# Performance work log

Hardware: AMD Instinct MI355X
Metric: run time of the kernel (lower is better)

The kernel has to match this reference:

```python
import jax, jax.numpy as jnp
import numpy as np

EMB_D, N_SLOTS, KEY_D, N_ITER = 768, 8, 128, 5
ATTN_EPS = 1e-8
LN_EPS = 1e-5


def layer_norm(x, g, b):
    mu = jnp.mean(x, axis=-1, keepdims=True)
    var = jnp.mean(jnp.square(x - mu), axis=-1, keepdims=True)
    return (x - mu) * jax.lax.rsqrt(var + LN_EPS) * g + b


def xavier(key, shape):
    fan_in, fan_out = shape[-1], shape[-2] if len(shape) > 1 else shape[-1]
    a = float(np.sqrt(6.0 / (fan_in + fan_out)))
    return jax.random.uniform(key, shape, jnp.float32, -a, a)


def setup_inputs() -> dict:
    key = jax.random.key(0)
    ks = jax.random.split(key, 24)
    B, N = 128, 196
    k = KEY_D
    inp = {
        "features": jax.random.normal(ks[0], (B, N, EMB_D), jnp.float32),
        "slot_noise": jax.random.normal(ks[1], (B, N_SLOTS, k), jnp.float32),
        # LayerNorms
        "ln_in_g": jnp.ones((EMB_D,), jnp.float32), "ln_in_b": jnp.zeros((EMB_D,), jnp.float32),
        "ln_slot_g": jnp.ones((k,), jnp.float32), "ln_slot_b": jnp.zeros((k,), jnp.float32),
        "ln_out_g": jnp.ones((k,), jnp.float32), "ln_out_b": jnp.zeros((k,), jnp.float32),
        "ln_dec_g": jnp.ones((k,), jnp.float32), "ln_dec_b": jnp.zeros((k,), jnp.float32),
        # slot prior
        "mu": xavier(ks[2], (1, 1, k)),
        "log_sigma": xavier(ks[3], (1, 1, k)),
        # projections (torch Linear weight layout: [out, in])
        "Wk": xavier(ks[4], (k, EMB_D)),
        "Wq": xavier(ks[5], (k, k)),
        "Wv": xavier(ks[6], (k, EMB_D)),
        # GRUCell
        "W_ih": jax.random.uniform(ks[7], (3 * k, k), jnp.float32, -1.0/np.sqrt(k), 1.0/np.sqrt(k)),
        "W_hh": jax.random.uniform(ks[8], (3 * k, k), jnp.float32, -1.0/np.sqrt(k), 1.0/np.sqrt(k)),
        "b_ih": jnp.zeros((3 * k,), jnp.float32),
        "b_hh": jnp.zeros((3 * k,), jnp.float32),
        # slot MLP
        "mlp_W1": xavier(ks[9], (k, k)), "mlp_b1": jnp.zeros((k,), jnp.float32),
        "mlp_W2": xavier(ks[10], (k, k)), "mlp_b2": jnp.zeros((k,), jnp.float32),
        # decoder
        "dec_W1": xavier(ks[11], (2 * k, k)), "dec_b1": jnp.zeros((2 * k,), jnp.float32),
        "dec_W2": xavier(ks[12], (EMB_D, 2 * k)), "dec_b2": jnp.zeros((EMB_D,), jnp.float32),
        "dec_W3": xavier(ks[13], (EMB_D, EMB_D)), "dec_b3": jnp.zeros((EMB_D,), jnp.float32),
    }
    return inp


def gru_cell(x, h, W_ih, W_hh, b_ih, b_hh):
    gi = x @ W_ih.T + b_ih  # [*, 3k]
    gh = h @ W_hh.T + b_hh
    ir, iz, inn = jnp.split(gi, 3, axis=-1)
    hr, hz, hn = jnp.split(gh, 3, axis=-1)
    r = jax.nn.sigmoid(ir + hr)
    z = jax.nn.sigmoid(iz + hz)
    n = jnp.tanh(inn + r * hn)
    return (1.0 - z) * n + z * h


def reference(features, slot_noise, ln_in_g, ln_in_b, ln_slot_g, ln_slot_b,
              ln_out_g, ln_out_b, ln_dec_g, ln_dec_b, mu, log_sigma,
              Wk, Wq, Wv, W_ih, W_hh, b_ih, b_hh,
              mlp_W1, mlp_b1, mlp_W2, mlp_b2,
              dec_W1, dec_b1, dec_W2, dec_b2, dec_W3, dec_b3):
    feats_ln = layer_norm(features, ln_in_g, ln_in_b)  # [B,N,E]
    slots = slot_noise * jnp.exp(log_sigma) + mu       # [B,K,D]
    k_proj = (feats_ln @ Wk.T) * (KEY_D ** -0.5)       # [B,N,D]
    v_proj = feats_ln @ Wv.T                           # [B,N,D]

    attn_vis = None
    for _ in range(N_ITER):
        slots_prev = slots
        s_ln = layer_norm(slots, ln_slot_g, ln_slot_b)
        q = s_ln @ Wq.T                                # [B,K,D]
        logits = jnp.einsum('bnd,bkd->bnk', k_proj, q)
        attn_vis = jax.nn.softmax(logits, axis=-1)     # softmax over slots
        attn = attn_vis + ATTN_EPS
        attn = attn / jnp.sum(attn, axis=-2, keepdims=True)  # normalize over tokens
        updates = jnp.einsum('bnk,bnd->bkd', attn, v_proj)
        slots = gru_cell(updates, slots_prev, W_ih, W_hh, b_ih, b_hh)
        h = jax.nn.relu(layer_norm(slots, ln_out_g, ln_out_b) @ mlp_W1.T + mlp_b1)
        slots = slots + (h @ mlp_W2.T + mlp_b2)

    sf = layer_norm(slots, ln_dec_g, ln_dec_b)
    sf = jax.nn.relu(sf @ dec_W1.T + dec_b1)
    sf = jax.nn.relu(sf @ dec_W2.T + dec_b2)
    sf = sf @ dec_W3.T + dec_b3                        # [B,K,E]
    recon = jnp.einsum('bkd,bnk->bnd', sf, attn_vis)   # [B,N,E]
    recon_loss = jnp.mean(jnp.square(recon - features))
    return slots, attn_vis, recon_loss
```

## Files before the change

kernel.cpp:

```cpp
#include <hip/hip_runtime.h>
#include <hip/hip_bf16.h>
#include <math.h>

#define B_    128
#define N_    196
#define E_    768
#define K_    8
#define D_    128
#define BNR   (B_*N_)
#define ITERS 5

#define OFF_PART   0
#define OFF_SDEC   512
#define OFF_WBF    66048
#define OFF_KPBF   647680
#define OFF_VPTBF  2351616
#define OFF_ABF    4186624

typedef __attribute__((ext_vector_type(8))) short bf16x8;
typedef __attribute__((ext_vector_type(4))) float f32x4;

#define MFMA16(a, b, c) __builtin_amdgcn_mfma_f32_16x16x32_bf16(a, b, c, 0, 0, 0)

__device__ __forceinline__ float wave_red_sum64(float v) {
    #pragma unroll
    for (int o = 32; o > 0; o >>= 1) v += __shfl_xor(v, o);
    return v;
}

__device__ __forceinline__ unsigned short f2bf(float v) {
    union { float f; unsigned int u; } c; c.f = v;
    unsigned int u = c.u + 0x7fffu + ((c.u >> 16) & 1u);
    return (unsigned short)(u >> 16);
}

__device__ __forceinline__ void gl_lds16(const void* g, void* l) {
    __builtin_amdgcn_global_load_lds(
        (const __attribute__((address_space(1))) unsigned int*)g,
        (__attribute__((address_space(3))) unsigned int*)l, 16, 0, 0);
}

__device__ __forceinline__ int swz128(int row, int j) {
    return row * 128 + ((((j >> 3) ^ (row & 7))) << 3) + (j & 7);
}
__device__ __forceinline__ int swz256(int row, int j) {
    return row * 256 + ((((j >> 3) ^ (row & 7))) << 3) + (j & 7);
}
__device__ __forceinline__ bf16x8 ldA128(const unsigned short* base, int fr, int kq, int ks) {
    int ch = (ks * 4 + kq) ^ (fr & 7);
    return *(const bf16x8*)(base + fr * 128 + ch * 8);
}
__device__ __forceinline__ bf16x8 ldA256(const unsigned short* base, int fr, int kq, int ks) {
    int ch = (ks * 4 + kq) ^ (fr & 7);
    return *(const bf16x8*)(base + fr * 256 + ch * 8);
}
__device__ __forceinline__ bf16x8 ldW128(const unsigned short* W, int row, int ks, int kq) {
    return *(const bf16x8*)(W + (size_t)row * 128 + ks * 32 + kq * 8);
}

struct WCEnt { const float* s; unsigned short* d; float scale; int t0; };
struct WCArgs { WCEnt m[10]; };

__global__ __launch_bounds__(256) void wconv_all(WCArgs a) {
    int bid = blockIdx.x, i = 0;
    #pragma unroll
    for (int j = 1; j < 10; ++j) if (bid >= a.m[j].t0) i = j;
    int off = (bid - a.m[i].t0) * 2048 + threadIdx.x * 8;
    const float* s = a.m[i].s + off;
    unsigned short* d = a.m[i].d + off;
    float sc = a.m[i].scale;
    float4 v0 = *(const float4*)s, v1 = *(const float4*)(s + 4);
    ushort4 o0, o1;
    o0.x = f2bf(v0.x * sc); o0.y = f2bf(v0.y * sc);
    o0.z = f2bf(v0.z * sc); o0.w = f2bf(v0.w * sc);
    o1.x = f2bf(v1.x * sc); o1.y = f2bf(v1.y * sc);
    o1.z = f2bf(v1.z * sc); o1.w = f2bf(v1.w * sc);
    *(ushort4*)d = o0; *(ushort4*)(d + 4) = o1;
}

__global__ __launch_bounds__(256) void padzero_k(unsigned short* kpb, unsigned short* vpt) {
    int i = blockIdx.x * 256 + threadIdx.x;
    ushort4 z = {0, 0, 0, 0};
    if (i < 49152) {
        int q = i * 4;
        int b = q / 1536, off = q - b * 1536;
        *(ushort4*)(kpb + ((size_t)b * 208 + 196) * 128 + off) = z;
    } else {
        int c = i - 49152;
        int bd = c / 7, cc = c - bd * 7;
        *(ushort4*)(vpt + (size_t)bd * 224 + 196 + cc * 4) = z;
    }
}

__global__ __launch_bounds__(256) void ln_bf16_k(const float* __restrict__ f,
                                                 const float* __restrict__ g,
                                                 const float* __restrict__ bv,
                                                 unsigned short* __restrict__ out) {
    int wid = blockIdx.x * 4 + (threadIdx.x >> 6);
    int lane = threadIdx.x & 63;
    const float* row = f + (size_t)wid * E_;
    float4 x[3];
    float s = 0.f, s2 = 0.f;
    #pragma unroll
    for (int c = 0; c < 3; ++c) {
        x[c] = *(const float4*)(row + c * 256 + lane * 4);
        s  += x[c].x + x[c].y + x[c].z + x[c].w;
        s2 += x[c].x * x[c].x + x[c].y * x[c].y + x[c].z * x[c].z + x[c].w * x[c].w;
    }
    s  = wave_red_sum64(s);
    s2 = wave_red_sum64(s2);
    float m = s * (1.f / E_);
    float rs = rsqrtf(s2 * (1.f / E_) - m * m + 1e-5f);
    #pragma unroll
    for (int c = 0; c < 3; ++c) {
        float4 g4 = *(const float4*)(g + c * 256 + lane * 4);
        float4 b4 = *(const float4*)(bv + c * 256 + lane * 4);
        ushort4 o;
        o.x = f2bf((x[c].x - m) * rs * g4.x + b4.x);
        o.y = f2bf((x[c].y - m) * rs * g4.y + b4.y);
        o.z = f2bf((x[c].z - m) * rs * g4.z + b4.z);
        o.w = f2bf((x[c].w - m) * rs * g4.w + b4.w);
        *(ushort4*)(out + (size_t)wid * E_ + c * 256 + lane * 4) = o;
    }
}

__global__ __launch_bounds__(256) void mfma_proj_k(const unsigned short* __restrict__ Abf,
                                                   const unsigned short* __restrict__ Wb,
                                                   unsigned short* __restrict__ kp_bf,
                                                   unsigned short* __restrict__ vpT_bf) {
    __shared__ __align__(16) unsigned short As[128 * 64];
    __shared__ __align__(16) unsigned short Bs[128 * 64];
    const int t = threadIdx.x, w = t >> 6, l = t & 63;
    const int m0 = blockIdx.x * 128;
    const int n0 = blockIdx.y * 128;
    const int wr = w >> 1, wc = w & 1;
    const int fr = l & 15, kq = l >> 4;
    f32x4 acc[4][4];
    #pragma unroll
    for (int mi = 0; mi < 4; ++mi)
        #pragma unroll
        for (int nj = 0; nj < 4; ++nj) acc[mi][nj] = (f32x4){0.f, 0.f, 0.f, 0.f};

    for (int ks = 0; ks < E_; ks += 64) {
        __syncthreads();
        #pragma unroll
        for (int j = 0; j < 4; ++j) {
            int ci = (w << 8) + (j << 6) + l;
            int r = ci >> 3, c = ci & 7;
            int cg = c ^ (r & 7);
            const unsigned short* ga = Abf + (size_t)(m0 + r) * E_ + ks + cg * 8;
            const unsigned short* gb = Wb  + (size_t)(n0 + r) * E_ + ks + cg * 8;
            gl_lds16(ga, As + (size_t)((w << 8) + (j << 6)) * 8);
            gl_lds16(gb, Bs + (size_t)((w << 8) + (j << 6)) * 8);
        }
        __syncthreads();
        #pragma unroll
        for (int kk = 0; kk < 2; ++kk) {
            bf16x8 af[4], bfr[4];
            int kci = kk * 4 + kq;
            int ch = kci ^ (fr & 7);
            #pragma unroll
            for (int mi = 0; mi < 4; ++mi)
                af[mi] = *(const bf16x8*)(As + (wr * 64 + mi * 16 + fr) * 64 + ch * 8);
            #pragma unroll
            for (int nj = 0; nj < 4; ++nj)
                bfr[nj] = *(const bf16x8*)(Bs + (wc * 64 + nj * 16 + fr) * 64 + ch * 8);
            #pragma unroll
            for (int mi = 0; mi < 4; ++mi)
                #pragma unroll
                for (int nj = 0; nj < 4; ++nj)
                    acc[mi][nj] = MFMA16(af[mi], bfr[nj], acc[mi][nj]);
        }
    }
    if (blockIdx.y == 0) {
        #pragma unroll
        for (int mi = 0; mi < 4; ++mi) {
            int rowbase = m0 + wr * 64 + mi * 16 + kq * 4;
            #pragma unroll
            for (int r = 0; r < 4; ++r) {
                int m = rowbase + r;
                int b = m / 196, rr = m - b * 196;
                size_t o = ((size_t)b * 208 + rr) * 128;
                #pragma unroll
                for (int nj = 0; nj < 4; ++nj)
                    kp_bf[o + wc * 64 + nj * 16 + fr] = f2bf(acc[mi][nj][r]);
            }
        }
    } else {
        #pragma unroll
        for (int mi = 0; mi < 4; ++mi) {
            int rowbase = m0 + wr * 64 + mi * 16 + kq * 4;
            #pragma unroll
            for (int r = 0; r < 4; ++r) {
                int m = rowbase + r;
                int b = m / 196, rr = m - b * 196;
                #pragma unroll
                for (int nj = 0; nj < 4; ++nj) {
                    int col = wc * 64 + nj * 16 + fr;
                    vpT_bf[((size_t)b * 128 + col) * 224 + rr] = f2bf(acc[mi][nj][r]);
                }
            }
        }
    }
}

template<int KTOT, int EPI>
__global__ __launch_bounds__(256) void mfma_mlp_k(const unsigned short* __restrict__ A,
                                                  const unsigned short* __restrict__ Bw,
                                                  const float* __restrict__ bias,
                                                  unsigned short* __restrict__ out_bf,
                                                  float* __restrict__ out_f,
                                                  int ldN) {
    __shared__ __align__(16) unsigned short As[128 * 64];
    __shared__ __align__(16) unsigned short Bs[128 * 64];
    const int t = threadIdx.x, w = t >> 6, l = t & 63;
    const int m0 = blockIdx.x * 128;
    const int n0 = blockIdx.y * 128;
    const int wr = w >> 1, wc = w & 1;
    const int fr = l & 15, kq = l >> 4;
    f32x4 acc[4][4];
    #pragma unroll
    for (int mi = 0; mi < 4; ++mi)
        #pragma unroll
        for (int nj = 0; nj < 4; ++nj) acc[mi][nj] = (f32x4){0.f, 0.f, 0.f, 0.f};

    for (int ks = 0; ks < KTOT; ks += 64) {
        __syncthreads();
        #pragma unroll
        for (int j = 0; j < 4; ++j) {
            int ci = (w << 8) + (j << 6) + l;
            int r = ci >> 3, c = ci & 7;
            int cg = c ^ (r & 7);
            gl_lds16(A  + (size_t)(m0 + r) * KTOT + ks + cg * 8,
                     As + (size_t)((w << 8) + (j << 6)) * 8);
            gl_lds16(Bw + (size_t)(n0 + r) * KTOT + ks + cg * 8,
                     Bs + (size_t)((w << 8) + (j << 6)) * 8);
        }
        __syncthreads();
        #pragma unroll
        for (int kk = 0; kk < 2; ++kk) {
            bf16x8 af[4], bfr[4];
            int ch = (kk * 4 + kq) ^ (fr & 7);
            #pragma unroll
            for (int mi = 0; mi < 4; ++mi)
                af[mi] = *(const bf16x8*)(As + (wr * 64 + mi * 16 + fr) * 64 + ch * 8);
            #pragma unroll
            for (int nj = 0; nj < 4; ++nj)
                bfr[nj] = *(const bf16x8*)(Bs + (wc * 64 + nj * 16 + fr) * 64 + ch * 8);
            #pragma unroll
            for (int mi = 0; mi < 4; ++mi)
                #pragma unroll
                for (int nj = 0; nj < 4; ++nj)
                    acc[mi][nj] = MFMA16(af[mi], bfr[nj], acc[mi][nj]);
        }
    }
    #pragma unroll
    for (int mi = 0; mi < 4; ++mi) {
        int rowbase = m0 + wr * 64 + mi * 16 + kq * 4;
        #pragma unroll
        for (int nj = 0; nj < 4; ++nj) {
            int col = n0 + wc * 64 + nj * 16 + fr;
            float bc = bias[col];
            #pragma unroll
            for (int r = 0; r < 4; ++r) {
                float v = acc[mi][nj][r] + bc;
                if (EPI == 0)
                    out_bf[(size_t)(rowbase + r) * ldN + col] = f2bf(fmaxf(v, 0.f));
                else
                    out_f[(size_t)(rowbase + r) * ldN + col] = v;
            }
        }
    }
}

__global__ __launch_bounds__(512) void slot_iter_mfma(
    const float* __restrict__ noise,
    const float* __restrict__ lsg, const float* __restrict__ lsb,
    const float* __restrict__ log_, const float* __restrict__ lob,
    const float* __restrict__ ldg_, const float* __restrict__ ldb_,
    const float* __restrict__ mup, const float* __restrict__ lsig,
    const unsigned short* __restrict__ Wq_bf,
    const unsigned short* __restrict__ Wih_bf,
    const unsigned short* __restrict__ Whh_bf,
    const float* __restrict__ bih, const float* __restrict__ bhh,
    const unsigned short* __restrict__ W1_bf, const float* __restrict__ mb1,
    const unsigned short* __restrict__ W2_bf, const float* __restrict__ mb2,
    const unsigned short* __restrict__ kp_bf,
    const unsigned short* __restrict__ vpT_bf,
    float* __restrict__ out_slots, float* __restrict__ out_attn,
    unsigned short* __restrict__ sdec_bf) {

    __shared__ float slots[8][128];
    __shared__ float attn[208][9];
    __shared__ float colsum[8];
    __shared__ __align__(16) unsigned short sln_bf[2048];
    __shared__ __align__(16) unsigned short q_bf[2048];
    __shared__ __align__(16) unsigned short upd_bf[2048];
    __shared__ __align__(16) unsigned short slots_bf[2048];
    __shared__ __align__(16) unsigned short h_bf[2048];
    __shared__ __align__(16) unsigned short attnT_bf[4096];

    const int b = blockIdx.x, t = threadIdx.x;
    const int lane = t & 63, w = t >> 6;
    const int fr = lane & 15, kq = lane >> 4;

    for (int i = t; i < 2048; i += 512) {
        sln_bf[i] = 0; q_bf[i] = 0; upd_bf[i] = 0; slots_bf[i] = 0; h_bf[i] = 0;
    }
    for (int i = t; i < 4096; i += 512) attnT_bf[i] = 0;

    for (int idx = t; idx < 1024; idx += 512) {
        int k = idx >> 7, d = idx & 127;
        float v = noise[(size_t)b * 1024 + idx] * expf(lsig[d]) + mup[d];
        slots[k][d] = v;
        slots_bf[swz128(k, d)] = f2bf(v);
    }
    __syncthreads();

    for (int it = 0; it < ITERS; ++it) {
        bool last = (it == ITERS - 1);
        {
            float x0 = slots[w][lane], x1 = slots[w][lane + 64];
            float s  = wave_red_sum64(x0 + x1);
            float s2 = wave_red_sum64(x0 * x0 + x1 * x1);
            float m = s * 0.0078125f;
            float rs = rsqrtf(s2 * 0.0078125f - m * m + 1e-5f);
            sln_bf[swz128(w, lane)]      = f2bf((x0 - m) * rs * lsg[lane]      + lsb[lane]);
            sln_bf[swz128(w, lane + 64)] = f2bf((x1 - m) * rs * lsg[lane + 64] + lsb[lane + 64]);
        }
        __syncthreads();
        {
            f32x4 acc = {0.f, 0.f, 0.f, 0.f};
            #pragma unroll
            for (int ks = 0; ks < 4; ++ks)
                acc = MFMA16(ldA128(sln_bf, fr, kq, ks), ldW128(Wq_bf, w * 16 + fr, ks, kq), acc);
            if (kq < 2) {
                #pragma unroll
                for (int r = 0; r < 4; ++r)
                    q_bf[swz128(kq * 4 + r, w * 16 + fr)] = f2bf(acc[r]);
            }
        }
        __syncthreads();
        #pragma unroll
        for (int p = 0; p < 2; ++p) {
            int tt = w + p * 8;
            if (tt <= 12) {
                f32x4 acc = {0.f, 0.f, 0.f, 0.f};
                const unsigned short* kpr = kp_bf + ((size_t)b * 208 + tt * 16 + fr) * 128;
                #pragma unroll
                for (int ks = 0; ks < 4; ++ks)
                    acc = MFMA16(*(const bf16x8*)(kpr + ks * 32 + kq * 8),
                                 ldA128(q_bf, fr, kq, ks), acc);
                #pragma unroll
                for (int r = 0; r < 4; ++r) {
                    float v = acc[r];
                    float mx = fmaxf(v, __shfl_xor(v, 1));
                    mx = fmaxf(mx, __shfl_xor(mx, 2));
                    mx = fmaxf(mx, __shfl_xor(mx, 4));
                    float e = expf(v - mx);
                    float sm = e;
                    sm += __shfl_xor(sm, 1); sm += __shfl_xor(sm, 2); sm += __shfl_xor(sm, 4);
                    int tok = tt * 16 + kq * 4 + r;
                    if (fr < 8 && tok < 196) attn[tok][fr] = e / sm;
                }
            }
        }
        __syncthreads();
        {
            float s = 0.f;
            for (int n = lane; n < 196; n += 64) s += attn[n][w];
            s = wave_red_sum64(s);
            if (lane == 0) colsum[w] = s + 196.0f * 1e-8f;
        }
        __syncthreads();
        for (int idx = t; idx < 1568; idx += 512) {
            int n = idx >> 3, k = idx & 7;
            float raw = attn[n][k];
            attnT_bf[swz256(k, n)] = f2bf((raw + 1e-8f) / colsum[k]);
            if (last) out_attn[((size_t)b * 196 + n) * 8 + k] = raw;
        }
        __syncthreads();
        {
            f32x4 acc = {0.f, 0.f, 0.f, 0.f};
            const unsigned short* vpr = vpT_bf + ((size_t)b * 128 + w * 16 + fr) * 224;
            #pragma unroll
            for (int ks = 0; ks < 7; ++ks)
                acc = MFMA16(ldA256(attnT_bf, fr, kq, ks),
                             *(const bf16x8*)(vpr + ks * 32 + kq * 8), acc);
            if (kq < 2) {
                #pragma unroll
                for (int r = 0; r < 4; ++r)
                    upd_bf[swz128(kq * 4 + r, w * 16 + fr)] = f2bf(acc[r]);
            }
        }
        __syncthreads();
        {
            f32x4 gi0 = {0,0,0,0}, gi1 = {0,0,0,0}, gi2 = {0,0,0,0};
            f32x4 gh0 = {0,0,0,0}, gh1 = {0,0,0,0}, gh2 = {0,0,0,0};
            #pragma unroll
            for (int ks = 0; ks < 4; ++ks) {
                bf16x8 au = ldA128(upd_bf,   fr, kq, ks);
                bf16x8 as = ldA128(slots_bf, fr, kq, ks);
                gi0 = MFMA16(au, ldW128(Wih_bf,       w * 16 + fr, ks, kq), gi0);
                gi1 = MFMA16(au, ldW128(Wih_bf, 128 + w * 16 + fr, ks, kq), gi1);
                gi2 = MFMA16(au, ldW128(Wih_bf, 256 + w * 16 + fr, ks, kq), gi2);
                gh0 = MFMA16(as, ldW128(Whh_bf,       w * 16 + fr, ks, kq), gh0);
                gh1 = MFMA16(as, ldW128(Whh_bf, 128 + w * 16 + fr, ks, kq), gh1);
                gh2 = MFMA16(as, ldW128(Whh_bf, 256 + w * 16 + fr, ks, kq), gh2);
            }
            __syncthreads();
            if (kq < 2) {
                int d = w * 16 + fr;
                float bi0 = bih[d], bi1 = bih[128 + d], bi2 = bih[256 + d];
                float bh0 = bhh[d], bh1 = bhh[128 + d], bh2 = bhh[256 + d];
                #pragma unroll
                for (int r = 0; r < 4; ++r) {
                    int m = kq * 4 + r;
                    float rr = 1.f / (1.f + expf(-((gi0[r] + bi0) + (gh0[r] + bh0))));
                    float zz = 1.f / (1.f + expf(-((gi1[r] + bi1) + (gh1[r] + bh1))));
                    float nn = tanhf((gi2[r] + bi2) + rr * (gh2[r] + bh2));
                    float h = slots[m][d];
                    float v = (1.f - zz) * nn + zz * h;
                    slots[m][d] = v;
                    slots_bf[swz128(m, d)] = f2bf(v);
                }
            }
        }
        __syncthreads();
        {
            float x0 = slots[w][lane], x1 = slots[w][lane + 64];
            float s  = wave_red_sum64(x0 + x1);
            float s2 = wave_red_sum64(x0 * x0 + x1 * x1);
            float m = s * 0.0078125f;
            float rs = rsqrtf(s2 * 0.0078125f - m * m + 1e-5f);
            sln_bf[swz128(w, lane)]      = f2bf((x0 - m) * rs * log_[lane]      + lob[lane]);
            sln_bf[swz128(w, lane + 64)] = f2bf((x1 - m) * rs * log_[lane + 64] + lob[lane + 64]);
        }
        __syncthreads();
        {
            f32x4 acc = {0.f, 0.f, 0.f, 0.f};
            #pragma unroll
            for (int ks = 0; ks < 4; ++ks)
                acc = MFMA16(ldA128(sln_bf, fr, kq, ks), ldW128(W1_bf, w * 16 + fr, ks, kq), acc);
            if (kq < 2) {
                float b1 = mb1[w * 16 + fr];
                #pragma unroll
                for (int r = 0; r < 4; ++r)
                    h_bf[swz128(kq * 4 + r, w * 16 + fr)] = f2bf(fmaxf(acc[r] + b1, 0.f));
            }
        }
        __syncthreads();
        {
            f32x4 acc = {0.f, 0.f, 0.f, 0.f};
            #pragma unroll
            for (int ks = 0; ks < 4; ++ks)
                acc = MFMA16(ldA128(h_bf, fr, kq, ks), ldW128(W2_bf, w * 16 + fr, ks, kq), acc);
            if (kq < 2) {
                float b2 = mb2[w * 16 + fr];
                #pragma unroll
                for (int r = 0; r < 4; ++r) {
                    int m = kq * 4 + r, d = w * 16 + fr;
                    float v = slots[m][d] + acc[r] + b2;
                    slots[m][d] = v;
                    slots_bf[swz128(m, d)] = f2bf(v);
                }
            }
        }
        __syncthreads();
    }
    {
        float x0 = slots[w][lane], x1 = slots[w][lane + 64];
        out_slots[(size_t)b * 1024 + w * 128 + lane]      = x0;
        out_slots[(size_t)b * 1024 + w * 128 + lane + 64] = x1;
        float s  = wave_red_sum64(x0 + x1);
        float s2 = wave_red_sum64(x0 * x0 + x1 * x1);
        float m = s * 0.0078125f;
        float rs = rsqrtf(s2 * 0.0078125f - m * m + 1e-5f);
        sdec_bf[((size_t)b * 8 + w) * 128 + lane]      = f2bf((x0 - m) * rs * ldg_[lane]      + ldb_[lane]);
        sdec_bf[((size_t)b * 8 + w) * 128 + lane + 64] = f2bf((x1 - m) * rs * ldg_[lane + 64] + ldb_[lane + 64]);
    }
}

__global__ __launch_bounds__(256) void recon_loss_k(
    const float* __restrict__ feats, const float* __restrict__ attnv,
    const float* __restrict__ sf, float* __restrict__ partials) {

    __shared__ float sfl[8][768];
    __shared__ float al[49][8];
    __shared__ float wred[4];
    int b = blockIdx.x, qd = blockIdx.y, t = threadIdx.x;
    for (int idx = t; idx < 8 * 768; idx += 256)
        ((float*)sfl)[idx] = sf[(size_t)b * 8 * 768 + idx];
    int n0 = qd * 49;
    for (int idx = t; idx < 49 * 8; idx += 256)
        ((float*)al)[idx] = attnv[((size_t)b * N_ + n0) * 8 + idx];
    __syncthreads();
    float acc = 0.f;
    for (int nl = 0; nl < 49; ++nl) {
        float a0 = al[nl][0], a1 = al[nl][1], a2 = al[nl][2], a3 = al[nl][3];
        float a4 = al[nl][4], a5 = al[nl][5], a6 = al[nl][6], a7 = al[nl][7];
        const float* frow = feats + ((size_t)(b * N_ + n0 + nl)) * E_;
        for (int c = t; c < E_; c += 256) {
            float r = sfl[0][c]*a0 + sfl[1][c]*a1 + sfl[2][c]*a2 + sfl[3][c]*a3
                    + sfl[4][c]*a4 + sfl[5][c]*a5 + sfl[6][c]*a6 + sfl[7][c]*a7;
            float d = r - frow[c];
            acc += d * d;
        }
    }
    acc = wave_red_sum64(acc);
    int lane = t & 63, w = t >> 6;
    if (lane == 0) wred[w] = acc;
    __syncthreads();
    if (t == 0) partials[b * 4 + qd] = wred[0] + wred[1] + wred[2] + wred[3];
}

__global__ __launch_bounds__(512) void loss_final_k(const float* __restrict__ partials,
                                                    float* __restrict__ out) {
    __shared__ float wred[8];
    int t = threadIdx.x;
    float v = partials[t];
    v = wave_red_sum64(v);
    if ((t & 63) == 0) wred[t >> 6] = v;
    __syncthreads();
    if (t == 0) {
        float s = 0.f;
        #pragma unroll
        for (int i = 0; i < 8; ++i) s += wred[i];
        out[0] = s / (float)(B_ * N_ * E_);
    }
}

extern "C" void kernel_launch(void* const* d_in, const int* in_sizes, int n_in,
                              void* d_out, int out_size, void* d_ws, size_t ws_size,
                              hipStream_t stream) {
    (void)in_sizes; (void)n_in; (void)out_size; (void)ws_size;
    const float* feats     = (const float*)d_in[0];
    const float* noise     = (const float*)d_in[1];
    const float* ln_in_g   = (const float*)d_in[2];
    const float* ln_in_b   = (const float*)d_in[3];
    const float* ln_slot_g = (const float*)d_in[4];
    const float* ln_slot_b = (const float*)d_in[5];
    const float* ln_out_g  = (const float*)d_in[6];
    const float* ln_out_b  = (const float*)d_in[7];
    const float* ln_dec_g  = (const float*)d_in[8];
    const float* ln_dec_b  = (const float*)d_in[9];
    const float* mu        = (const float*)d_in[10];
    const float* log_sigma = (const float*)d_in[11];
    const float* Wk        = (const float*)d_in[12];
    const float* Wq        = (const float*)d_in[13];
    const float* Wv        = (const float*)d_in[14];
    const float* W_ih      = (const float*)d_in[15];
    const float* W_hh      = (const float*)d_in[16];
    const float* b_ih      = (const float*)d_in[17];
    const float* b_hh      = (const float*)d_in[18];
    const float* mlp_W1    = (const float*)d_in[19];
    const float* mlp_b1    = (const float*)d_in[20];
    const float* mlp_W2    = (const float*)d_in[21];
    const float* mlp_b2    = (const float*)d_in[22];
    const float* dec_W1    = (const float*)d_in[23];
    const float* dec_b1    = (const float*)d_in[24];
    const float* dec_W2    = (const float*)d_in[25];
    const float* dec_b2    = (const float*)d_in[26];
    const float* dec_W3    = (const float*)d_in[27];
    const float* dec_b3    = (const float*)d_in[28];

    float* ws    = (float*)d_ws;
    float* parts = ws + OFF_PART;
    unsigned short* sdec_bf = (unsigned short*)(ws + OFF_SDEC);
    unsigned short* Wb      = (unsigned short*)(ws + OFF_WBF);
    unsigned short* Wq_bf   = Wb + 196608;
    unsigned short* Wih_bf  = Wb + 212992;
    unsigned short* Whh_bf  = Wb + 262144;
    unsigned short* W1_bf   = Wb + 311296;
    unsigned short* W2_bf   = Wb + 327680;
    unsigned short* dW1_bf  = Wb + 344064;
    unsigned short* dW2_bf  = Wb + 376832;
    unsigned short* dW3_bf  = Wb + 573440;
    unsigned short* kp_bf   = (unsigned short*)(ws + OFF_KPBF);
    unsigned short* vpT_bf  = (unsigned short*)(ws + OFF_VPTBF);
    unsigned short* Abf     = (unsigned short*)(ws + OFF_ABF);
    float*          sf      = ws + OFF_ABF;
    unsigned short* h1_bf   = (unsigned short*)(ws + OFF_ABF + 786432);
    unsigned short* h2_bf   = (unsigned short*)(ws + OFF_ABF + 786432 + 131072);

    float* out_slots = (float*)d_out;
    float* out_attn  = out_slots + 131072;
    float* out_loss  = out_slots + 331776;

    WCArgs wa;
    wa.m[0] = {Wk,     Wb,      0.08838834764831845f, 0};
    wa.m[1] = {Wv,     Wb + 98304, 1.f,               48};
    wa.m[2] = {Wq,     Wq_bf,   1.f,                  96};
    wa.m[3] = {W_ih,   Wih_bf,  1.f,                  104};
    wa.m[4] = {W_hh,   Whh_bf,  1.f,                  128};
    wa.m[5] = {mlp_W1, W1_bf,   1.f,                  152};
    wa.m[6] = {mlp_W2, W2_bf,   1.f,                  160};
    wa.m[7] = {dec_W1, dW1_bf,  1.f,                  168};
    wa.m[8] = {dec_W2, dW2_bf,  1.f,                  184};
    wa.m[9] = {dec_W3, dW3_bf,  1.f,                  280};
    wconv_all<<<568, 256, 0, stream>>>(wa);

    padzero_k<<<640, 256, 0, stream>>>(kp_bf, vpT_bf);
    ln_bf16_k<<<BNR / 4, 256, 0, stream>>>(feats, ln_in_g, ln_in_b, Abf);
    mfma_proj_k<<<dim3(BNR / 128, 2), 256, 0, stream>>>(Abf, Wb, kp_bf, vpT_bf);

    slot_iter_mfma<<<B_, 512, 0, stream>>>(noise, ln_slot_g, ln_slot_b, ln_out_g, ln_out_b,
                                           ln_dec_g, ln_dec_b, mu, log_sigma,
                                           Wq_bf, Wih_bf, Whh_bf, b_ih, b_hh,
                                           W1_bf, mlp_b1, W2_bf, mlp_b2, kp_bf, vpT_bf,
                                           out_slots, out_attn, sdec_bf);

    mfma_mlp_k<128, 0><<<dim3(8, 2), 256, 0, stream>>>(sdec_bf, dW1_bf, dec_b1, h1_bf, nullptr, 256);
    mfma_mlp_k<256, 0><<<dim3(8, 6), 256, 0, stream>>>(h1_bf,  dW2_bf, dec_b2, h2_bf, nullptr, 768);
    mfma_mlp_k<768, 1><<<dim3(8, 6), 256, 0, stream>>>(h2_bf,  dW3_bf, dec_b3, nullptr, sf, 768);

    recon_loss_k<<<dim3(B_, 4), 256, 0, stream>>>(feats, out_attn, sf, parts);
    loss_final_k<<<1, 512, 0, stream>>>(parts, out_loss);
}
```

Measured before the change: 202.5 us.

## Fold Wq into key projection and fuse column-sum into softmax pass

Precomputes (Wq^T·Wk·scale) so the key projection yields keys already multiplied by Wq. The per-iteration q projection GEMM and its barrier disappear from the slot loop. Attention column sums are accumulated inside the softmax pass rather than in a separate reduction with its own barrier, and weight conversion is merged with pad zeroing into one launch. A GRU barrier and the slots_bf write are removed. Folding the weights adds one more bf16 rounding step, which may shift accuracy slightly.

```diff
diff --git a/kernel.cpp b/kernel.cpp
--- a/kernel.cpp
+++ b/kernel.cpp
@@ -13,9 +13,9 @@
 #define OFF_PART   0
 #define OFF_SDEC   512
 #define OFF_WBF    66048
-#define OFF_KPBF   647680
-#define OFF_VPTBF  2351616
-#define OFF_ABF    4186624
+#define OFF_KPBF   639488
+#define OFF_VPTBF  2343424
+#define OFF_ABF    4178432
 
 typedef __attribute__((ext_vector_type(8))) short bf16x8;
 typedef __attribute__((ext_vector_type(4))) float f32x4;
@@ -46,49 +46,96 @@
 __device__ __forceinline__ int swz256(int row, int j) {
     return row * 256 + ((((j >> 3) ^ (row & 7))) << 3) + (j & 7);
 }
-__device__ __forceinline__ bf16x8 ldA128(const unsigned short* base, int fr, int kq, int ks) {
-    int ch = (ks * 4 + kq) ^ (fr & 7);
-    return *(const bf16x8*)(base + fr * 128 + ch * 8);
-}
-__device__ __forceinline__ bf16x8 ldA256(const unsigned short* base, int fr, int kq, int ks) {
-    int ch = (ks * 4 + kq) ^ (fr & 7);
-    return *(const bf16x8*)(base + fr * 256 + ch * 8);
+__device__ __forceinline__ bf16x8 ldA128(const unsigned short* base, int row, int kq, int ks) {
+    int ch = (ks * 4 + kq) ^ (row & 7);
+    return *(const bf16x8*)(base + row * 128 + ch * 8);
+}
+__device__ __forceinline__ bf16x8 ldA256(const unsigned short* base, int row, int kq, int ks) {
+    int ch = (ks * 4 + kq) ^ (row & 7);
+    return *(const bf16x8*)(base + row * 256 + ch * 8);
 }
 __device__ __forceinline__ bf16x8 ldW128(const unsigned short* W, int row, int ks, int kq) {
     return *(const bf16x8*)(W + (size_t)row * 128 + ks * 32 + kq * 8);
 }
 
-struct WCEnt { const float* s; unsigned short* d; float scale; int t0; };
-struct WCArgs { WCEnt m[10]; };
-
-__global__ __launch_bounds__(256) void wconv_all(WCArgs a) {
-    int bid = blockIdx.x, i = 0;
-    #pragma unroll
-    for (int j = 1; j < 10; ++j) if (bid >= a.m[j].t0) i = j;
-    int off = (bid - a.m[i].t0) * 2048 + threadIdx.x * 8;
-    const float* s = a.m[i].s + off;
-    unsigned short* d = a.m[i].d + off;
-    float sc = a.m[i].scale;
-    float4 v0 = *(const float4*)s, v1 = *(const float4*)(s + 4);
-    ushort4 o0, o1;
-    o0.x = f2bf(v0.x * sc); o0.y = f2bf(v0.y * sc);
-    o0.z = f2bf(v0.z * sc); o0.w = f2bf(v0.w * sc);
-    o1.x = f2bf(v1.x * sc); o1.y = f2bf(v1.y * sc);
-    o1.z = f2bf(v1.z * sc); o1.w = f2bf(v1.w * sc);
-    *(ushort4*)d = o0; *(ushort4*)(d + 4) = o1;
-}
-
-__global__ __launch_bounds__(256) void padzero_k(unsigned short* kpb, unsigned short* vpt) {
-    int i = blockIdx.x * 256 + threadIdx.x;
-    ushort4 z = {0, 0, 0, 0};
-    if (i < 49152) {
-        int q = i * 4;
-        int b = q / 1536, off = q - b * 1536;
-        *(ushort4*)(kpb + ((size_t)b * 208 + 196) * 128 + off) = z;
+__global__ __launch_bounds__(256) void wfold_k(const float* __restrict__ Wq,
+                                               const float* __restrict__ Wk,
+                                               unsigned short* __restrict__ WMt) {
+    __shared__ __align__(16) unsigned short Aq[128 * 128];
+    __shared__ __align__(16) unsigned short Bk[128 * 128];
+    const float s = 0.08838834764831845f;
+    int t = threadIdx.x;
+    int e0 = blockIdx.x * 128;
+    for (int idx = t; idx < 16384; idx += 256) {
+        int o = idx >> 7, c = idx & 127;
+        Aq[swz128(c, o)] = f2bf(Wq[(size_t)o * 128 + c]);
+        Bk[swz128(c, o)] = f2bf(Wk[(size_t)o * 768 + e0 + c] * s);
+    }
+    __syncthreads();
+    int w = t >> 6, l = t & 63;
+    int wr = w >> 1, wc = w & 1, fr = l & 15, kq = l >> 4;
+    f32x4 acc[4][4];
+    #pragma unroll
+    for (int mi = 0; mi < 4; ++mi)
+        #pragma unroll
+        for (int nj = 0; nj < 4; ++nj) acc[mi][nj] = (f32x4){0.f, 0.f, 0.f, 0.f};
+    #pragma unroll
+    for (int ks = 0; ks < 4; ++ks) {
+        bf16x8 af[4], bfr[4];
+        #pragma unroll
+        for (int mi = 0; mi < 4; ++mi) af[mi] = ldA128(Aq, wr * 64 + mi * 16 + fr, kq, ks);
+        #pragma unroll
+        for (int nj = 0; nj < 4; ++nj) bfr[nj] = ldA128(Bk, wc * 64 + nj * 16 + fr, kq, ks);
+        #pragma unroll
+        for (int mi = 0; mi < 4; ++mi)
+            #pragma unroll
+            for (int nj = 0; nj < 4; ++nj)
+                acc[mi][nj] = MFMA16(af[mi], bfr[nj], acc[mi][nj]);
+    }
+    #pragma unroll
+    for (int mi = 0; mi < 4; ++mi) {
+        int rowbase = wr * 64 + mi * 16 + kq * 4;
+        #pragma unroll
+        for (int nj = 0; nj < 4; ++nj) {
+            int col = e0 + wc * 64 + nj * 16 + fr;
+            #pragma unroll
+            for (int r = 0; r < 4; ++r)
+                WMt[(size_t)(rowbase + r) * 768 + col] = f2bf(acc[mi][nj][r]);
+        }
+    }
+}
+
+struct WCEnt { const float* s; unsigned short* d; int t0; };
+struct WCArgs { WCEnt m[8]; };
+
+__global__ __launch_bounds__(256) void wprep_k(WCArgs a,
+                                               unsigned short* __restrict__ kpb,
+                                               unsigned short* __restrict__ vpt) {
+    int bid = blockIdx.x;
+    if (bid < 512) {
+        int i = 0;
+        #pragma unroll
+        for (int j = 1; j < 8; ++j) if (bid >= a.m[j].t0) i = j;
+        int off = (bid - a.m[i].t0) * 2048 + threadIdx.x * 8;
+        const float* s = a.m[i].s + off;
+        unsigned short* d = a.m[i].d + off;
+        float4 v0 = *(const float4*)s, v1 = *(const float4*)(s + 4);
+        ushort4 o0, o1;
+        o0.x = f2bf(v0.x); o0.y = f2bf(v0.y); o0.z = f2bf(v0.z); o0.w = f2bf(v0.w);
+        o1.x = f2bf(v1.x); o1.y = f2bf(v1.y); o1.z = f2bf(v1.z); o1.w = f2bf(v1.w);
+        *(ushort4*)d = o0; *(ushort4*)(d + 4) = o1;
     } else {
-        int c = i - 49152;
-        int bd = c / 7, cc = c - bd * 7;
-        *(ushort4*)(vpt + (size_t)bd * 224 + 196 + cc * 4) = z;
+        int i = (bid - 512) * 256 + threadIdx.x;
+        ushort4 z = {0, 0, 0, 0};
+        if (i < 49152) {
+            int q = i * 4;
+            int b = q / 1536, off = q - b * 1536;
+            *(ushort4*)(kpb + ((size_t)b * 208 + 196) * 128 + off) = z;
+        } else {
+            int c = i - 49152;
+            int bd = c / 7, cc = c - bd * 7;
+            *(ushort4*)(vpt + (size_t)bd * 224 + 196 + cc * 4) = z;
+        }
     }
 }
 
@@ -125,14 +172,15 @@
 }
 
 __global__ __launch_bounds__(256) void mfma_proj_k(const unsigned short* __restrict__ Abf,
-                                                   const unsigned short* __restrict__ Wb,
-                                                   unsigned short* __restrict__ kp_bf,
+                                                   const unsigned short* __restrict__ WMt,
+                                                   const unsigned short* __restrict__ Wv_bf,
+                                                   unsigned short* __restrict__ kpq_bf,
                                                    unsigned short* __restrict__ vpT_bf) {
     __shared__ __align__(16) unsigned short As[128 * 64];
     __shared__ __align__(16) unsigned short Bs[128 * 64];
     const int t = threadIdx.x, w = t >> 6, l = t & 63;
     const int m0 = blockIdx.x * 128;
-    const int n0 = blockIdx.y * 128;
+    const unsigned short* Wbase = (blockIdx.y == 0) ? WMt : Wv_bf;
     const int wr = w >> 1, wc = w & 1;
     const int fr = l & 15, kq = l >> 4;
     f32x4 acc[4][4];
@@ -148,17 +196,16 @@
             int ci = (w << 8) + (j << 6) + l;
             int r = ci >> 3, c = ci & 7;
             int cg = c ^ (r & 7);
-            const unsigned short* ga = Abf + (size_t)(m0 + r) * E_ + ks + cg * 8;
-            const unsigned short* gb = Wb  + (size_t)(n0 + r) * E_ + ks + cg * 8;
-            gl_lds16(ga, As + (size_t)((w << 8) + (j << 6)) * 8);
-            gl_lds16(gb, Bs + (size_t)((w << 8) + (j << 6)) * 8);
+            gl_lds16(Abf   + (size_t)(m0 + r) * E_ + ks + cg * 8,
+                     As + (size_t)((w << 8) + (j << 6)) * 8);
+            gl_lds16(Wbase + (size_t)r * E_ + ks + cg * 8,
+                     Bs + (size_t)((w << 8) + (j << 6)) * 8);
         }
         __syncthreads();
         #pragma unroll
         for (int kk = 0; kk < 2; ++kk) {
             bf16x8 af[4], bfr[4];
-            int kci = kk * 4 + kq;
-            int ch = kci ^ (fr & 7);
+            int ch = (kk * 4 + kq) ^ (fr & 7);
             #pragma unroll
             for (int mi = 0; mi < 4; ++mi)
                 af[mi] = *(const bf16x8*)(As + (wr * 64 + mi * 16 + fr) * 64 + ch * 8);
@@ -183,7 +230,7 @@
                 size_t o = ((size_t)b * 208 + rr) * 128;
                 #pragma unroll
                 for (int nj = 0; nj < 4; ++nj)
-                    kp_bf[o + wc * 64 + nj * 16 + fr] = f2bf(acc[mi][nj][r]);
+                    kpq_bf[o + wc * 64 + nj * 16 + fr] = f2bf(acc[mi][nj][r]);
             }
         }
     } else {
@@ -279,22 +326,20 @@
     const float* __restrict__ log_, const float* __restrict__ lob,
     const float* __restrict__ ldg_, const float* __restrict__ ldb_,
     const float* __restrict__ mup, const float* __restrict__ lsig,
-    const unsigned short* __restrict__ Wq_bf,
     const unsigned short* __restrict__ Wih_bf,
     const unsigned short* __restrict__ Whh_bf,
     const float* __restrict__ bih, const float* __restrict__ bhh,
     const unsigned short* __restrict__ W1_bf, const float* __restrict__ mb1,
     const unsigned short* __restrict__ W2_bf, const float* __restrict__ mb2,
-    const unsigned short* __restrict__ kp_bf,
+    const unsigned short* __restrict__ kpq_bf,
     const unsigned short* __restrict__ vpT_bf,
     float* __restrict__ out_slots, float* __restrict__ out_attn,
     unsigned short* __restrict__ sdec_bf) {
 
     __shared__ float slots[8][128];
     __shared__ float attn[208][9];
-    __shared__ float colsum[8];
+    __shared__ float colpart[8][8];
     __shared__ __align__(16) unsigned short sln_bf[2048];
-    __shared__ __align__(16) unsigned short q_bf[2048];
     __shared__ __align__(16) unsigned short upd_bf[2048];
     __shared__ __align__(16) unsigned short slots_bf[2048];
     __shared__ __align__(16) unsigned short h_bf[2048];
@@ -305,7 +350,7 @@
     const int fr = lane & 15, kq = lane >> 4;
 
     for (int i = t; i < 2048; i += 512) {
-        sln_bf[i] = 0; q_bf[i] = 0; upd_bf[i] = 0; slots_bf[i] = 0; h_bf[i] = 0;
+        sln_bf[i] = 0; upd_bf[i] = 0; slots_bf[i] = 0; h_bf[i] = 0;
     }
     for (int i = t; i < 4096; i += 512) attnT_bf[i] = 0;
 
@@ -330,54 +375,51 @@
         }
         __syncthreads();
         {
-            f32x4 acc = {0.f, 0.f, 0.f, 0.f};
-            #pragma unroll
-            for (int ks = 0; ks < 4; ++ks)
-                acc = MFMA16(ldA128(sln_bf, fr, kq, ks), ldW128(Wq_bf, w * 16 + fr, ks, kq), acc);
-            if (kq < 2) {
-                #pragma unroll
-                for (int r = 0; r < 4; ++r)
-                    q_bf[swz128(kq * 4 + r, w * 16 + fr)] = f2bf(acc[r]);
-            }
-        }
-        __syncthreads();
-        #pragma unroll
-        for (int p = 0; p < 2; ++p) {
-            int tt = w + p * 8;
-            if (tt <= 12) {
-                f32x4 acc = {0.f, 0.f, 0.f, 0.f};
-                const unsigned short* kpr = kp_bf + ((size_t)b * 208 + tt * 16 + fr) * 128;
-                #pragma unroll
-                for (int ks = 0; ks < 4; ++ks)
-                    acc = MFMA16(*(const bf16x8*)(kpr + ks * 32 + kq * 8),
-                                 ldA128(q_bf, fr, kq, ks), acc);
-                #pragma unroll
-                for (int r = 0; r < 4; ++r) {
-                    float v = acc[r];
-                    float mx = fmaxf(v, __shfl_xor(v, 1));
-                    mx = fmaxf(mx, __shfl_xor(mx, 2));
-                    mx = fmaxf(mx, __shfl_xor(mx, 4));
-                    float e = expf(v - mx);
-                    float sm = e;
-                    sm += __shfl_xor(sm, 1); sm += __shfl_xor(sm, 2); sm += __shfl_xor(sm, 4);
-                    int tok = tt * 16 + kq * 4 + r;
-                    if (fr < 8 && tok < 196) attn[tok][fr] = e / sm;
+            float cp = 0.f;
+            #pragma unroll
+            for (int p = 0; p < 2; ++p) {
+                int tt = w + p * 8;
+                if (tt <= 12) {
+                    f32x4 acc = {0.f, 0.f, 0.f, 0.f};
+                    const unsigned short* kpr = kpq_bf + ((size_t)b * 208 + tt * 16 + fr) * 128;
+                    #pragma unroll
+                    for (int ks = 0; ks < 4; ++ks)
+                        acc = MFMA16(*(const bf16x8*)(kpr + ks * 32 + kq * 8),
+                                     ldA128(sln_bf, fr, kq, ks), acc);
+                    #pragma unroll
+                    for (int r = 0; r < 4; ++r) {
+                        float v = acc[r];
+                        float mx = fmaxf(v, __shfl_xor(v, 1));
+                        mx = fmaxf(mx, __shfl_xor(mx, 2));
+                        mx = fmaxf(mx, __shfl_xor(mx, 4));
+                        float e = expf(v - mx);
+                        float sm = e;
+                        sm += __shfl_xor(sm, 1); sm += __shfl_xor(sm, 2); sm += __shfl_xor(sm, 4);
+                        float a = e / sm;
+                        int tok = tt * 16 + kq * 4 + r;
+                        bool valid = (tok < 196);
+                        if (fr < 8 && valid) attn[tok][fr] = a;
+                        cp += valid ? a : 0.f;
+                    }
                 }
             }
-        }
-        __syncthreads();
-        {
-            float s = 0.f;
-            for (int n = lane; n < 196; n += 64) s += attn[n][w];
-            s = wave_red_sum64(s);
-            if (lane == 0) colsum[w] = s + 196.0f * 1e-8f;
-        }
-        __syncthreads();
-        for (int idx = t; idx < 1568; idx += 512) {
-            int n = idx >> 3, k = idx & 7;
-            float raw = attn[n][k];
-            attnT_bf[swz256(k, n)] = f2bf((raw + 1e-8f) / colsum[k]);
-            if (last) out_attn[((size_t)b * 196 + n) * 8 + k] = raw;
+            cp += __shfl_xor(cp, 16);
+            cp += __shfl_xor(cp, 32);
+            if (lane < 8) colpart[w][lane] = cp;
+        }
+        __syncthreads();
+        {
+            int k = t & 7;
+            float cs = colpart[0][k] + colpart[1][k] + colpart[2][k] + colpart[3][k]
+                     + colpart[4][k] + colpart[5][k] + colpart[6][k] + colpart[7][k]
+                     + 196.0f * 1e-8f;
+            float inv = 1.f / cs;
+            for (int idx = t; idx < 1568; idx += 512) {
+                int n = idx >> 3;
+                float raw = attn[n][k];
+                attnT_bf[swz256(k, n)] = f2bf((raw + 1e-8f) * inv);
+                if (last) out_attn[((size_t)b * 196 + n) * 8 + k] = raw;
+            }
         }
         __syncthreads();
         {
@@ -408,7 +450,6 @@
                 gh1 = MFMA16(as, ldW128(Whh_bf, 128 + w * 16 + fr, ks, kq), gh1);
                 gh2 = MFMA16(as, ldW128(Whh_bf, 256 + w * 16 + fr, ks, kq), gh2);
             }
-            __syncthreads();
             if (kq < 2) {
                 int d = w * 16 + fr;
                 float bi0 = bih[d], bi1 = bih[128 + d], bi2 = bih[256 + d];
@@ -420,9 +461,7 @@
                     float zz = 1.f / (1.f + expf(-((gi1[r] + bi1) + (gh1[r] + bh1))));
                     float nn = tanhf((gi2[r] + bi2) + rr * (gh2[r] + bh2));
                     float h = slots[m][d];
-                    float v = (1.f - zz) * nn + zz * h;
-                    slots[m][d] = v;
-                    slots_bf[swz128(m, d)] = f2bf(v);
+                    slots[m][d] = (1.f - zz) * nn + zz * h;
                 }
             }
         }
@@ -567,16 +606,17 @@
     float* ws    = (float*)d_ws;
     float* parts = ws + OFF_PART;
     unsigned short* sdec_bf = (unsigned short*)(ws + OFF_SDEC);
-    unsigned short* Wb      = (unsigned short*)(ws + OFF_WBF);
-    unsigned short* Wq_bf   = Wb + 196608;
-    unsigned short* Wih_bf  = Wb + 212992;
-    unsigned short* Whh_bf  = Wb + 262144;
-    unsigned short* W1_bf   = Wb + 311296;
-    unsigned short* W2_bf   = Wb + 327680;
-    unsigned short* dW1_bf  = Wb + 344064;
-    unsigned short* dW2_bf  = Wb + 376832;
-    unsigned short* dW3_bf  = Wb + 573440;
-    unsigned short* kp_bf   = (unsigned short*)(ws + OFF_KPBF);
+    unsigned short* Wbase   = (unsigned short*)(ws + OFF_WBF);
+    unsigned short* Wv_bf   = Wbase;
+    unsigned short* Wih_bf  = Wbase + 98304;
+    unsigned short* Whh_bf  = Wbase + 147456;
+    unsigned short* W1_bf   = Wbase + 196608;
+    unsigned short* W2_bf   = Wbase + 212992;
+    unsigned short* dW1_bf  = Wbase + 229376;
+    unsigned short* dW2_bf  = Wbase + 262144;
+    unsigned short* dW3_bf  = Wbase + 458752;
+    unsigned short* WMt     = Wbase + 1048576;
+    unsigned short* kpq_bf  = (unsigned short*)(ws + OFF_KPBF);
     unsigned short* vpT_bf  = (unsigned short*)(ws + OFF_VPTBF);
     unsigned short* Abf     = (unsigned short*)(ws + OFF_ABF);
     float*          sf      = ws + OFF_ABF;
@@ -587,27 +627,26 @@
     float* out_attn  = out_slots + 131072;
     float* out_loss  = out_slots + 331776;
 
+    wfold_k<<<6, 256, 0, stream>>>(Wq, Wk, WMt);
+
     WCArgs wa;
-    wa.m[0] = {Wk,     Wb,      0.08838834764831845f, 0};
-    wa.m[1] = {Wv,     Wb + 98304, 1.f,               48};
-    wa.m[2] = {Wq,     Wq_bf,   1.f,                  96};
-    wa.m[3] = {W_ih,   Wih_bf,  1.f,                  104};
-    wa.m[4] = {W_hh,   Whh_bf,  1.f,                  128};
-    wa.m[5] = {mlp_W1, W1_bf,   1.f,                  152};
-    wa.m[6] = {mlp_W2, W2_bf,   1.f,                  160};
-    wa.m[7] = {dec_W1, dW1_bf,  1.f,                  168};
-    wa.m[8] = {dec_W2, dW2_bf,  1.f,                  184};
-    wa.m[9] = {dec_W3, dW3_bf,  1.f,                  280};
-    wconv_all<<<568, 256, 0, stream>>>(wa);
-
-    padzero_k<<<640, 256, 0, stream>>>(kp_bf, vpT_bf);
+    wa.m[0] = {Wv,     Wv_bf,  0};
+    wa.m[1] = {W_ih,   Wih_bf, 48};
+    wa.m[2] = {W_hh,   Whh_bf, 72};
+    wa.m[3] = {mlp_W1, W1_bf,  96};
+    wa.m[4] = {mlp_W2, W2_bf,  104};
+    wa.m[5] = {dec_W1, dW1_bf, 112};
+    wa.m[6] = {dec_W2, dW2_bf, 128};
+    wa.m[7] = {dec_W3, dW3_bf, 224};
+    wprep_k<<<1152, 256, 0, stream>>>(wa, kpq_bf, vpT_bf);
+
     ln_bf16_k<<<BNR / 4, 256, 0, stream>>>(feats, ln_in_g, ln_in_b, Abf);
-    mfma_proj_k<<<dim3(BNR / 128, 2), 256, 0, stream>>>(Abf, Wb, kp_bf, vpT_bf);
+    mfma_proj_k<<<dim3(BNR / 128, 2), 256, 0, stream>>>(Abf, WMt, Wv_bf, kpq_bf, vpT_bf);
 
     slot_iter_mfma<<<B_, 512, 0, stream>>>(noise, ln_slot_g, ln_slot_b, ln_out_g, ln_out_b,
                                            ln_dec_g, ln_dec_b, mu, log_sigma,
-                                           Wq_bf, Wih_bf, Whh_bf, b_ih, b_hh,
-                                           W1_bf, mlp_b1, W2_bf, mlp_b2, kp_bf, vpT_bf,
+                                           Wih_bf, Whh_bf, b_ih, b_hh,
+                                           W1_bf, mlp_b1, W2_bf, mlp_b2, kpq_bf, vpT_bf,
                                            out_slots, out_attn, sdec_bf);
 
     mfma_mlp_k<128, 0><<<dim3(8, 2), 256, 0, stream>>>(sdec_bf, dW1_bf, dec_b1, h1_bf, nullptr, 256);
```

After: 200.9 us. No clear change (-0.8%).
